# Performance work log

Measured on AMD Instinct MI355X. Metric: run time of the kernel, lower is better.

The kernel has to match this reference:

```python
import jax, jax.numpy as jnp
import numpy as np
import math

D_MODEL = 1024
N_HEADS = 16
HEAD_DIM = D_MODEL // N_HEADS

def setup_inputs() -> dict:
    key = jax.random.key(0)
    k1, k2, k3 = jax.random.split(key, 3)
    B, T = 4, 2048
    x = jax.random.normal(k1, (B, T, D_MODEL), dtype=jnp.float32)
    # weights stored as [in, out]; equivalent to torch Linear weight.T
    w_qkv = jax.random.normal(k2, (D_MODEL, 3 * D_MODEL), dtype=jnp.float32) * (1.0 / math.sqrt(D_MODEL))
    w_proj = jax.random.normal(k3, (D_MODEL, D_MODEL), dtype=jnp.float32) * (1.0 / math.sqrt(D_MODEL))
    return {"x": x, "w_qkv": w_qkv, "w_proj": w_proj}

def reference(x, w_qkv, w_proj):
    B, T, C = x.shape
    qkv = x @ w_qkv  # [B,T,3C]
    q, k, v = jnp.split(qkv, 3, axis=-1)
    # [B,T,C] -> [B,H,T,Dh]
    def to_heads(t):
        return t.reshape(B, T, N_HEADS, HEAD_DIM).transpose(0, 2, 1, 3)
    q, k, v = to_heads(q), to_heads(k), to_heads(v)
    scale = 1.0 / math.sqrt(HEAD_DIM)
    att = jnp.einsum('bhqd,bhkd->bhqk', q, k) * scale  # [B,H,T,T]
    causal = jnp.tril(jnp.ones((T, T), dtype=bool))
    att = jnp.where(causal[None, None], att, -jnp.inf)
    att = jax.nn.softmax(att, axis=-1)
    y = jnp.einsum('bhqk,bhkd->bhqd', att, v)  # [B,H,T,Dh]
    y = y.transpose(0, 2, 1, 3).reshape(B, T, C)
    return y @ w_proj
```

## Files before the change

### kernel.cpp

```cpp
#include <hip/hip_runtime.h>
#include <hip/hip_bf16.h>

typedef __bf16 bf16x8 __attribute__((ext_vector_type(8)));
typedef __bf16 bf16x4 __attribute__((ext_vector_type(4)));
typedef float  f32x4  __attribute__((ext_vector_type(4)));

#define MFMA16(a,b,c) __builtin_amdgcn_mfma_f32_16x16x32_bf16((a),(b),(c),0,0,0)

#define T_SEQ 2048
#define CDIM  1024
#define NH    16
#define DH    64
#define C3    3072
#define QKS   2048

#define GLDS(g, l) __builtin_amdgcn_global_load_lds( \
    (const __attribute__((address_space(1))) void*)(g), \
    (__attribute__((address_space(3))) void*)(l), 16, 0, 0)

__global__ void cast_f32_bf16_kernel(const float* __restrict__ in,
                                     __bf16* __restrict__ out, int n4) {
  int i = blockIdx.x * 256 + threadIdx.x;
  if (i >= n4) return;
  f32x4 v = ((const f32x4*)in)[i];
  bf16x4 o;
  o[0] = (__bf16)v[0]; o[1] = (__bf16)v[1];
  o[2] = (__bf16)v[2]; o[3] = (__bf16)v[3];
  ((bf16x4*)out)[i] = o;
}

__global__ void transpose_cast_kernel(const float* __restrict__ W,
                                      __bf16* __restrict__ WT, int R, int C,
                                      float qscale, int qcols) {
  __shared__ float tile[32][33];
  int c0 = blockIdx.x * 32, r0 = blockIdx.y * 32;
  int tx = threadIdx.x, ty = threadIdx.y;
#pragma unroll
  for (int i = 0; i < 32; i += 8)
    tile[ty + i][tx] = W[(size_t)(r0 + ty + i) * C + c0 + tx];
  __syncthreads();
#pragma unroll
  for (int i = 0; i < 32; i += 8) {
    int c = c0 + ty + i;
    float sc = (c < qcols) ? qscale : 1.0f;
    WT[(size_t)c * R + r0 + tx] = (__bf16)(tile[tx][ty + i] * sc);
  }
}

__global__ __launch_bounds__(256, 2)
void gemm1_kernel(const __bf16* __restrict__ A, const __bf16* __restrict__ BT,
                  __bf16* __restrict__ qkp, __bf16* __restrict__ VTp) {
  __shared__ __align__(16) __bf16 S[2][2][128 * 64];
  const int K = 1024;
  const int tid  = threadIdx.x;
  const int lane = tid & 63;
  const int g    = lane >> 4;
  const int l16  = lane & 15;
  const int wave = tid >> 6;
  const int wm   = wave >> 1;
  const int wn   = wave & 1;

  const int sb = (blockIdx.x & 7) * 192 + (blockIdx.x >> 3);
  const int bn = sb % 24;
  const int bm = sb / 24;

  const int srow = tid >> 3;
  const int scol = ((tid & 7) << 4) ^ ((srow & 7) << 4);
  const int swz  = (l16 & 7) << 4;

  const __bf16* Abase = A  + (size_t)(bm * 128 + srow) * K + (scol >> 1);
  const __bf16* Bbase = BT + (size_t)(bn * 128 + srow) * K + (scol >> 1);

  f32x4  acc[4][4] = {};
  bf16x8 ar[2][2];
  bf16x8 br[4][2];

#define STAGE_A(BUF, K0) do { \
    _Pragma("unroll") for (int u_ = 0; u_ < 4; ++u_) \
      GLDS(Abase + (size_t)u_ * 32 * K + (K0), (char*)&S[BUF][0][0] + u_ * 4096 + tid * 16); \
  } while (0)
#define STAGE_B(BUF, K0) do { \
    _Pragma("unroll") for (int u_ = 0; u_ < 4; ++u_) \
      GLDS(Bbase + (size_t)u_ * 32 * K + (K0), (char*)&S[BUF][1][0] + u_ * 4096 + tid * 16); \
  } while (0)

#define LDA(BUF, IH) do { \
    const char* ab_ = (const char*)&S[BUF][0][0]; \
    _Pragma("unroll") for (int i_ = 0; i_ < 2; ++i_) { \
      const char* rp_ = ab_ + (wm * 64 + (IH) * 32 + i_ * 16 + l16) * 128; \
      _Pragma("unroll") for (int kk_ = 0; kk_ < 2; ++kk_) \
        ar[i_][kk_] = *(const bf16x8*)(rp_ + ((kk_ * 64 + g * 16) ^ swz)); \
    } \
  } while (0)

#define LDB(BUF) do { \
    const char* bb_ = (const char*)&S[BUF][1][0]; \
    _Pragma("unroll") for (int j_ = 0; j_ < 4; ++j_) { \
      const char* rp_ = bb_ + (wn * 64 + j_ * 16 + l16) * 128; \
      _Pragma("unroll") for (int kk_ = 0; kk_ < 2; ++kk_) \
        br[j_][kk_] = *(const bf16x8*)(rp_ + ((kk_ * 64 + g * 16) ^ swz)); \
    } \
  } while (0)

#define MQ(IH) do { \
    __builtin_amdgcn_s_setprio(1); \
    _Pragma("unroll") for (int kk_ = 0; kk_ < 2; ++kk_) \
      _Pragma("unroll") for (int i_ = 0; i_ < 2; ++i_) \
        _Pragma("unroll") for (int j_ = 0; j_ < 4; ++j_) \
          acc[(IH) * 2 + i_][j_] = \
              MFMA16(ar[i_][kk_], br[j_][kk_], acc[(IH) * 2 + i_][j_]); \
    __builtin_amdgcn_s_setprio(0); \
  } while (0)

#define SBAR do { \
    __builtin_amdgcn_sched_barrier(0); \
    __builtin_amdgcn_s_barrier(); \
    __builtin_amdgcn_sched_barrier(0); \
  } while (0)

  STAGE_A(0, 0); STAGE_B(0, 0);
  asm volatile("s_waitcnt vmcnt(0)" ::: "memory");
  SBAR;

  const int NIT = K >> 7;
#pragma unroll 1
  for (int it = 0; it < NIT; ++it) {
    const int kt1 = (2 * it + 1) << 6;
    const int kt2 = (2 * it + 2) << 6;
    const bool stg = (it + 1) < NIT;

    LDA(0, 0); LDB(0);
    STAGE_A(1, kt1); STAGE_B(1, kt1);
    SBAR; MQ(0); SBAR;

    LDA(0, 1);
    asm volatile("s_waitcnt vmcnt(0)" ::: "memory");
    SBAR; MQ(1); SBAR;

    LDA(1, 0); LDB(1);
    if (stg) { STAGE_A(0, kt2); STAGE_B(0, kt2); }
    SBAR; MQ(0); SBAR;

    LDA(1, 1);
    asm volatile("s_waitcnt vmcnt(0)" ::: "memory");
    SBAR; MQ(1); SBAR;
  }

  if (bn < 16) {
#pragma unroll
    for (int a = 0; a < 4; ++a) {
      const int row0 = bm * 128 + wm * 64 + a * 16 + g * 4;
#pragma unroll
      for (int jj = 0; jj < 4; ++jj) {
        const int col = bn * 128 + wn * 64 + jj * 16 + l16;
#pragma unroll
        for (int r = 0; r < 4; ++r)
          qkp[(size_t)(row0 + r) * QKS + col] = (__bf16)acc[a][jj][r];
      }
    }
  } else {
#pragma unroll
    for (int a = 0; a < 4; ++a) {
      const int row0 = bm * 128 + wm * 64 + a * 16 + g * 4;
      const int b    = row0 >> 11;
      const int t0   = row0 & 2047;
#pragma unroll
      for (int jj = 0; jj < 4; ++jj) {
        const int c = (bn - 16) * 128 + wn * 64 + jj * 16 + l16;
        bf16x4 pb;
#pragma unroll
        for (int r = 0; r < 4; ++r) pb[r] = (__bf16)acc[a][jj][r];
        *(bf16x4*)(VTp + ((size_t)((b << 10) + c)) * T_SEQ + t0) = pb;
      }
    }
  }
#undef STAGE_A
#undef STAGE_B
#undef LDA
#undef LDB
#undef MQ
#undef SBAR
}

__global__ __launch_bounds__(512, 1)
void gemm2_kernel(const __bf16* __restrict__ A, const __bf16* __restrict__ BT,
                  float* __restrict__ Cout) {
  __shared__ __align__(16) __bf16 S[2][3][128 * 64];
  const int tid  = threadIdx.x;
  const int lane = tid & 63;
  const int g    = lane >> 4;
  const int l16  = lane & 15;
  const int wave = tid >> 6;
  const int wm   = wave >> 2;
  const int wn   = wave & 3;

  const int K = 1024;
  const int sb = (blockIdx.x & 7) * 32 + (blockIdx.x >> 3);
  const int bn = sb & 7;
  const int bm = sb >> 3;

  const int srow = tid >> 3;
  const int scol = ((tid & 7) << 4) ^ ((srow & 7) << 4);
  const int swz  = (l16 & 7) << 4;

  const __bf16* Abase = A  + (size_t)(bm * 256 + srow) * K + (scol >> 1);
  const __bf16* Bbase = BT + (size_t)(bn * 128 + srow) * K + (scol >> 1);

  f32x4  acc[8][2] = {};
  bf16x8 ar[4][2];
  bf16x8 br[2][2];

#define STAGE2(BUF, U, K0) do { \
    const __bf16* sp_ = ((U) < 2 ? Abase + (size_t)(U) * 128 * K : Bbase) + (K0); \
    char* dp_ = (char*)&S[BUF][U][0] + tid * 16; \
    GLDS(sp_, dp_); \
    GLDS(sp_ + (size_t)64 * K, dp_ + 8192); \
  } while (0)

#define LDA2(BUF, MH) do { \
    const char* ab_ = (const char*)&S[BUF][wm][0]; \
    _Pragma("unroll") for (int i_ = 0; i_ < 4; ++i_) { \
      const char* rp_ = ab_ + ((MH) * 64 + i_ * 16 + l16) * 128; \
      _Pragma("unroll") for (int kk_ = 0; kk_ < 2; ++kk_) \
        ar[i_][kk_] = *(const bf16x8*)(rp_ + ((kk_ * 64 + g * 16) ^ swz)); \
    } \
  } while (0)

#define LDB2(BUF) do { \
    const char* bb_ = (const char*)&S[BUF][2][0]; \
    _Pragma("unroll") for (int j_ = 0; j_ < 2; ++j_) { \
      const char* rp_ = bb_ + (wn * 32 + j_ * 16 + l16) * 128; \
      _Pragma("unroll") for (int kk_ = 0; kk_ < 2; ++kk_) \
        br[j_][kk_] = *(const bf16x8*)(rp_ + ((kk_ * 64 + g * 16) ^ swz)); \
    } \
  } while (0)

#define MQ2(MH) do { \
    __builtin_amdgcn_s_setprio(1); \
    _Pragma("unroll") for (int kk_ = 0; kk_ < 2; ++kk_) \
      _Pragma("unroll") for (int i_ = 0; i_ < 4; ++i_) \
        _Pragma("unroll") for (int j_ = 0; j_ < 2; ++j_) \
          acc[(MH) * 4 + i_][j_] = \
              MFMA16(ar[i_][kk_], br[j_][kk_], acc[(MH) * 4 + i_][j_]); \
    __builtin_amdgcn_s_setprio(0); \
  } while (0)

#define SBAR2 do { \
    __builtin_amdgcn_sched_barrier(0); \
    __builtin_amdgcn_s_barrier(); \
    __builtin_amdgcn_sched_barrier(0); \
  } while (0)

  STAGE2(0, 0, 0); STAGE2(0, 1, 0); STAGE2(0, 2, 0);
  STAGE2(1, 0, 64);
  asm volatile("s_waitcnt vmcnt(2)" ::: "memory");
  SBAR2;

  const int NIT = K >> 7;
#pragma unroll 1
  for (int it = 0; it < NIT; ++it) {
    const int k1 = (2 * it + 1) << 6;
    const int k2 = (2 * it + 2) << 6;
    const int k3 = (2 * it + 3) << 6;
    const bool stg = (it + 1) < NIT;

    LDA2(0, 0); LDB2(0);
    STAGE2(1, 1, k1); STAGE2(1, 2, k1);
    SBAR2; MQ2(0); SBAR2;

    LDA2(0, 1);
    if (stg) {
      STAGE2(0, 0, k2);
      asm volatile("s_waitcnt vmcnt(2)" ::: "memory");
    } else {
      asm volatile("s_waitcnt vmcnt(0)" ::: "memory");
    }
    SBAR2; MQ2(1); SBAR2;

    LDA2(1, 0); LDB2(1);
    if (stg) { STAGE2(0, 1, k2); STAGE2(0, 2, k2); }
    SBAR2; MQ2(0); SBAR2;

    LDA2(1, 1);
    if (stg) {
      STAGE2(1, 0, k3);
      asm volatile("s_waitcnt vmcnt(2)" ::: "memory");
    }
    SBAR2; MQ2(1); SBAR2;
  }

#pragma unroll
  for (int ii = 0; ii < 8; ++ii) {
    const int row0 = bm * 256 + wm * 128 + ii * 16 + g * 4;
#pragma unroll
    for (int jj = 0; jj < 2; ++jj) {
      const int col = bn * 128 + wn * 32 + jj * 16 + l16;
#pragma unroll
      for (int r = 0; r < 4; ++r)
        Cout[(size_t)(row0 + r) * 1024 + col] = acc[ii][jj][r];
    }
  }
#undef STAGE2
#undef LDA2
#undef LDB2
#undef MQ2
#undef SBAR2
}

__global__ __launch_bounds__(256)
void attn_kernel(const __bf16* __restrict__ qk, const __bf16* __restrict__ VT,
                 __bf16* __restrict__ y) {
  __shared__ __align__(16) __bf16 Klds[2][64 * 64];
  __shared__ __align__(16) __bf16 Vlds[2][64 * 64];
  __shared__ __align__(16) __bf16 Plds[4][32 * 64];
  const int tid  = threadIdx.x;
  const int lane = tid & 63;
  const int g    = lane >> 4;
  const int l16  = lane & 15;
  const int wave = tid >> 6;

  const int pairid = blockIdx.x >> 6;
  const int bh     = blockIdx.x & 63;
  const int h      = bh & (NH - 1);
  const int b      = bh >> 4;

  const __bf16* Qg = qk + (size_t)b * T_SEQ * QKS + h * DH;
  const __bf16* Kg = Qg + 1024;
  const __bf16* Vt = VT + ((size_t)(b << 10) + h * DH) * T_SEQ;

  const int srow = tid >> 3;
  const int scol = ((tid & 7) * 16) ^ ((srow & 7) << 4);
  const int swz  = (l16 & 7) << 4;

  const float NEG = -3.0e38f;

  bf16x8 ones;
#pragma unroll
  for (int j = 0; j < 8; ++j) ones[j] = (__bf16)1.0f;

  char* Pw = (char*)&Plds[wave][0];

#pragma unroll 1
  for (int ph = 0; ph < 2; ++ph) {
    const int qt    = ph ? (15 - pairid) : pairid;
    const int qbase = qt * 128 + wave * 32;

    bf16x8 qf[2][2];
#pragma unroll
    for (int qg = 0; qg < 2; ++qg)
#pragma unroll
      for (int kk = 0; kk < 2; ++kk)
        qf[qg][kk] = *(const bf16x8*)(Qg + (size_t)(qbase + qg * 16 + l16) * QKS + kk * 32 + g * 8);

    f32x4 o[2][4] = {};
    f32x4 o_l[2]  = {};

    const int nkb = 2 * qt + 2;
    {
      const __bf16* ksrc = Kg + (size_t)srow * QKS + (scol >> 1);
      GLDS(ksrc, (char*)&Klds[0][0] + tid * 16);
      GLDS(ksrc + (size_t)32 * QKS, (char*)&Klds[0][0] + 4096 + tid * 16);
      const __bf16* vsrc = Vt + (size_t)srow * T_SEQ + (scol >> 1);
      GLDS(vsrc, (char*)&Vlds[0][0] + tid * 16);
      GLDS(vsrc + (size_t)32 * T_SEQ, (char*)&Vlds[0][0] + 4096 + tid * 16);
    }
    __syncthreads();

    const __bf16* kstage = Kg + (size_t)(64 + srow) * QKS + (scol >> 1);
    const __bf16* vstage = Vt + (size_t)srow * T_SEQ + 64 + (scol >> 1);

#pragma unroll 1
    for (int kb = 0; kb < nkb; ++kb) {
      const int cur = kb & 1;
      if (kb + 1 < nkb) {
        GLDS(kstage, (char*)&Klds[cur ^ 1][0] + tid * 16);
        GLDS(kstage + (size_t)32 * QKS, (char*)&Klds[cur ^ 1][0] + 4096 + tid * 16);
        GLDS(vstage, (char*)&Vlds[cur ^ 1][0] + tid * 16);
        GLDS(vstage + (size_t)32 * T_SEQ, (char*)&Vlds[cur ^ 1][0] + 4096 + tid * 16);
        kstage += (size_t)64 * QKS;
        vstage += 64;
      }

      f32x4 s[2][4] = {};
      const char* Kb = (const char*)&Klds[cur][0];
#pragma unroll
      for (int kk = 0; kk < 2; ++kk) {
#pragma unroll
        for (int st = 0; st < 4; ++st) {
          const char* rowp = Kb + (st * 16 + l16) * 128;
          bf16x8 kf = *(const bf16x8*)(rowp + ((kk * 64 + g * 16) ^ swz));
          s[0][st] = MFMA16(kf, qf[0][kk], s[0][st]);
          s[1][st] = MFMA16(kf, qf[1][kk], s[1][st]);
        }
      }
      if (kb >= 2 * qt) {
        const int kvbase = (kb - 2 * qt) * 64;
#pragma unroll
        for (int qg = 0; qg < 2; ++qg) {
          const int qloc = wave * 32 + qg * 16 + l16;
#pragma unroll
          for (int st = 0; st < 4; ++st)
#pragma unroll
            for (int r = 0; r < 4; ++r)
              if (kvbase + st * 16 + g * 4 + r > qloc) s[qg][st][r] = NEG;
        }
      }
#pragma unroll
      for (int qg = 0; qg < 2; ++qg) {
        char* Pr = Pw + (qg * 16 + l16) * 128;
#pragma unroll
        for (int st = 0; st < 4; ++st) {
          bf16x4 pb;
#pragma unroll
          for (int r = 0; r < 4; ++r)
            pb[r] = (__bf16)__builtin_amdgcn_exp2f(s[qg][st][r]);
          *(bf16x4*)(Pr + ((st * 32 + g * 8) ^ swz)) = pb;
        }
      }

      const char* Vb = (const char*)&Vlds[cur][0];
#pragma unroll
      for (int hf = 0; hf < 2; ++hf) {
        bf16x8 pf0 = *(const bf16x8*)(Pw + (l16)       * 128 + ((hf * 64 + g * 16) ^ swz));
        bf16x8 pf1 = *(const bf16x8*)(Pw + (16 + l16)  * 128 + ((hf * 64 + g * 16) ^ swz));
        o_l[0] = MFMA16(ones, pf0, o_l[0]);
        o_l[1] = MFMA16(ones, pf1, o_l[1]);
#pragma unroll
        for (int dt = 0; dt < 4; ++dt) {
          bf16x8 vf = *(const bf16x8*)(Vb + (dt * 16 + l16) * 128 + ((hf * 64 + g * 16) ^ swz));
          o[0][dt] = MFMA16(vf, pf0, o[0][dt]);
          o[1][dt] = MFMA16(vf, pf1, o[1][dt]);
        }
      }
      __syncthreads();
    }

#pragma unroll
    for (int qg = 0; qg < 2; ++qg) {
      const float inv_l = 1.0f / o_l[qg][0];
      const int qrow = qbase + qg * 16 + l16;
#pragma unroll
      for (int dt = 0; dt < 4; ++dt)
#pragma unroll
        for (int r = 0; r < 4; ++r)
          y[((size_t)b * T_SEQ + qrow) * CDIM + h * DH + dt * 16 + g * 4 + r] =
              (__bf16)(o[qg][dt][r] * inv_l);
    }
  }
}

extern "C" void kernel_launch(void* const* d_in, const int* in_sizes, int n_in,
                              void* d_out, int out_size, void* d_ws, size_t ws_size,
                              hipStream_t stream) {
  const float* x      = (const float*)d_in[0];
  const float* w_qkv  = (const float*)d_in[1];
  const float* w_proj = (const float*)d_in[2];
  float* out = (float*)d_out;

  __bf16* xb     = (__bf16*)d_ws;
  __bf16* wqkvT  = xb + 8388608;
  __bf16* wprojT = wqkvT + 3145728;
  __bf16* qk     = wprojT + 1048576;
  __bf16* VT     = qk + 16777216;
  __bf16* yb     = VT + 8388608;

  const float SCF = 0.125f * 1.44269504088896340736f;

  cast_f32_bf16_kernel<<<8192, 256, 0, stream>>>(x, xb, 2097152);
  transpose_cast_kernel<<<dim3(96, 32), dim3(32, 8), 0, stream>>>(w_qkv, wqkvT, 1024, 3072, SCF, 1024);
  transpose_cast_kernel<<<dim3(32, 32), dim3(32, 8), 0, stream>>>(w_proj, wprojT, 1024, 1024, 1.0f, 0);
  gemm1_kernel<<<1536, 256, 0, stream>>>(xb, wqkvT, qk, VT);
  attn_kernel<<<512, 256, 0, stream>>>(qk, VT, yb);
  gemm2_kernel<<<256, 512, 0, stream>>>(yb, wprojT, out);
}
```

Baseline: 153.9 us.

## Software-pipeline attention loop: overlap QK/softmax of next block with PV of previous

Restructures the attention inner loop so that each iteration computes QK^T and exp for key block kb while doing the P·V product for block kb-1. V gets a triple buffer and P a per-wave double buffer so the two stages do not overwrite each other's data. The aim is to interleave the exp/VALU work with the MFMA work and hide LDS latency. In exchange it adds LDS usage (more shared memory per block, possibly lower occupancy) and a prologue/epilogue with extra barriers.

```diff
diff --git a/kernel.cpp b/kernel.cpp
--- a/kernel.cpp
+++ b/kernel.cpp
@@ -311,8 +311,8 @@
 void attn_kernel(const __bf16* __restrict__ qk, const __bf16* __restrict__ VT,
                  __bf16* __restrict__ y) {
   __shared__ __align__(16) __bf16 Klds[2][64 * 64];
-  __shared__ __align__(16) __bf16 Vlds[2][64 * 64];
-  __shared__ __align__(16) __bf16 Plds[4][32 * 64];
+  __shared__ __align__(16) __bf16 Vlds[3][64 * 64];
+  __shared__ __align__(16) __bf16 Plds[4][2][32 * 64];
   const int tid  = threadIdx.x;
   const int lane = tid & 63;
   const int g    = lane >> 4;
@@ -338,7 +338,62 @@
 #pragma unroll
   for (int j = 0; j < 8; ++j) ones[j] = (__bf16)1.0f;
 
-  char* Pw = (char*)&Plds[wave][0];
+#define STAGE_KV(T, KB, VB) do { \
+    const __bf16* ks_ = Kg + (size_t)((T) * 64 + srow) * QKS + (scol >> 1); \
+    GLDS(ks_, (char*)&Klds[KB][0] + tid * 16); \
+    GLDS(ks_ + (size_t)32 * QKS, (char*)&Klds[KB][0] + 4096 + tid * 16); \
+    const __bf16* vs_ = Vt + (size_t)srow * T_SEQ + (T) * 64 + (scol >> 1); \
+    GLDS(vs_, (char*)&Vlds[VB][0] + tid * 16); \
+    GLDS(vs_ + (size_t)32 * T_SEQ, (char*)&Vlds[VB][0] + 4096 + tid * 16); \
+  } while (0)
+
+#define QKSM(KB, PS, KB_IDX, QT) do { \
+    f32x4 s[2][4] = {}; \
+    const char* Kb_ = (const char*)&Klds[KB][0]; \
+    _Pragma("unroll") for (int kk = 0; kk < 2; ++kk) { \
+      _Pragma("unroll") for (int st = 0; st < 4; ++st) { \
+        const char* rowp = Kb_ + (st * 16 + l16) * 128; \
+        bf16x8 kf = *(const bf16x8*)(rowp + ((kk * 64 + g * 16) ^ swz)); \
+        s[0][st] = MFMA16(kf, qf[0][kk], s[0][st]); \
+        s[1][st] = MFMA16(kf, qf[1][kk], s[1][st]); \
+      } \
+    } \
+    if ((KB_IDX) >= 2 * (QT)) { \
+      const int kvbase = ((KB_IDX) - 2 * (QT)) * 64; \
+      _Pragma("unroll") for (int qg = 0; qg < 2; ++qg) { \
+        const int qloc = wave * 32 + qg * 16 + l16; \
+        _Pragma("unroll") for (int st = 0; st < 4; ++st) \
+          _Pragma("unroll") for (int r = 0; r < 4; ++r) \
+            if (kvbase + st * 16 + g * 4 + r > qloc) s[qg][st][r] = NEG; \
+      } \
+    } \
+    char* Pw_ = (char*)&Plds[wave][PS][0]; \
+    _Pragma("unroll") for (int qg = 0; qg < 2; ++qg) { \
+      char* Pr_ = Pw_ + (qg * 16 + l16) * 128; \
+      _Pragma("unroll") for (int st = 0; st < 4; ++st) { \
+        bf16x4 pb; \
+        _Pragma("unroll") for (int r = 0; r < 4; ++r) \
+          pb[r] = (__bf16)__builtin_amdgcn_exp2f(s[qg][st][r]); \
+        *(bf16x4*)(Pr_ + ((st * 32 + g * 8) ^ swz)) = pb; \
+      } \
+    } \
+  } while (0)
+
+#define PV(VB, PS) do { \
+    const char* Vb_ = (const char*)&Vlds[VB][0]; \
+    const char* Pw_ = (const char*)&Plds[wave][PS][0]; \
+    _Pragma("unroll") for (int hf = 0; hf < 2; ++hf) { \
+      bf16x8 pf0 = *(const bf16x8*)(Pw_ + (l16)      * 128 + ((hf * 64 + g * 16) ^ swz)); \
+      bf16x8 pf1 = *(const bf16x8*)(Pw_ + (16 + l16) * 128 + ((hf * 64 + g * 16) ^ swz)); \
+      o_l[0] = MFMA16(ones, pf0, o_l[0]); \
+      o_l[1] = MFMA16(ones, pf1, o_l[1]); \
+      _Pragma("unroll") for (int dt = 0; dt < 4; ++dt) { \
+        bf16x8 vf = *(const bf16x8*)(Vb_ + (dt * 16 + l16) * 128 + ((hf * 64 + g * 16) ^ swz)); \
+        o[0][dt] = MFMA16(vf, pf0, o[0][dt]); \
+        o[1][dt] = MFMA16(vf, pf1, o[1][dt]); \
+      } \
+    } \
+  } while (0)
 
 #pragma unroll 1
   for (int ph = 0; ph < 2; ++ph) {
@@ -356,84 +411,22 @@
     f32x4 o_l[2]  = {};
 
     const int nkb = 2 * qt + 2;
-    {
-      const __bf16* ksrc = Kg + (size_t)srow * QKS + (scol >> 1);
-      GLDS(ksrc, (char*)&Klds[0][0] + tid * 16);
-      GLDS(ksrc + (size_t)32 * QKS, (char*)&Klds[0][0] + 4096 + tid * 16);
-      const __bf16* vsrc = Vt + (size_t)srow * T_SEQ + (scol >> 1);
-      GLDS(vsrc, (char*)&Vlds[0][0] + tid * 16);
-      GLDS(vsrc + (size_t)32 * T_SEQ, (char*)&Vlds[0][0] + 4096 + tid * 16);
-    }
+
     __syncthreads();
-
-    const __bf16* kstage = Kg + (size_t)(64 + srow) * QKS + (scol >> 1);
-    const __bf16* vstage = Vt + (size_t)srow * T_SEQ + 64 + (scol >> 1);
+    STAGE_KV(0, 0, 0);
+    __syncthreads();
+    if (nkb > 1) STAGE_KV(1, 1, 1);
+    QKSM(0, 0, 0, qt);
+    __syncthreads();
 
 #pragma unroll 1
-    for (int kb = 0; kb < nkb; ++kb) {
-      const int cur = kb & 1;
-      if (kb + 1 < nkb) {
-        GLDS(kstage, (char*)&Klds[cur ^ 1][0] + tid * 16);
-        GLDS(kstage + (size_t)32 * QKS, (char*)&Klds[cur ^ 1][0] + 4096 + tid * 16);
-        GLDS(vstage, (char*)&Vlds[cur ^ 1][0] + tid * 16);
-        GLDS(vstage + (size_t)32 * T_SEQ, (char*)&Vlds[cur ^ 1][0] + 4096 + tid * 16);
-        kstage += (size_t)64 * QKS;
-        vstage += 64;
-      }
-
-      f32x4 s[2][4] = {};
-      const char* Kb = (const char*)&Klds[cur][0];
-#pragma unroll
-      for (int kk = 0; kk < 2; ++kk) {
-#pragma unroll
-        for (int st = 0; st < 4; ++st) {
-          const char* rowp = Kb + (st * 16 + l16) * 128;
-          bf16x8 kf = *(const bf16x8*)(rowp + ((kk * 64 + g * 16) ^ swz));
-          s[0][st] = MFMA16(kf, qf[0][kk], s[0][st]);
-          s[1][st] = MFMA16(kf, qf[1][kk], s[1][st]);
-        }
-      }
-      if (kb >= 2 * qt) {
-        const int kvbase = (kb - 2 * qt) * 64;
-#pragma unroll
-        for (int qg = 0; qg < 2; ++qg) {
-          const int qloc = wave * 32 + qg * 16 + l16;
-#pragma unroll
-          for (int st = 0; st < 4; ++st)
-#pragma unroll
-            for (int r = 0; r < 4; ++r)
-              if (kvbase + st * 16 + g * 4 + r > qloc) s[qg][st][r] = NEG;
-        }
-      }
-#pragma unroll
-      for (int qg = 0; qg < 2; ++qg) {
-        char* Pr = Pw + (qg * 16 + l16) * 128;
-#pragma unroll
-        for (int st = 0; st < 4; ++st) {
-          bf16x4 pb;
-#pragma unroll
-          for (int r = 0; r < 4; ++r)
-            pb[r] = (__bf16)__builtin_amdgcn_exp2f(s[qg][st][r]);
-          *(bf16x4*)(Pr + ((st * 32 + g * 8) ^ swz)) = pb;
-        }
-      }
-
-      const char* Vb = (const char*)&Vlds[cur][0];
-#pragma unroll
-      for (int hf = 0; hf < 2; ++hf) {
-        bf16x8 pf0 = *(const bf16x8*)(Pw + (l16)       * 128 + ((hf * 64 + g * 16) ^ swz));
-        bf16x8 pf1 = *(const bf16x8*)(Pw + (16 + l16)  * 128 + ((hf * 64 + g * 16) ^ swz));
-        o_l[0] = MFMA16(ones, pf0, o_l[0]);
-        o_l[1] = MFMA16(ones, pf1, o_l[1]);
-#pragma unroll
-        for (int dt = 0; dt < 4; ++dt) {
-          bf16x8 vf = *(const bf16x8*)(Vb + (dt * 16 + l16) * 128 + ((hf * 64 + g * 16) ^ swz));
-          o[0][dt] = MFMA16(vf, pf0, o[0][dt]);
-          o[1][dt] = MFMA16(vf, pf1, o[1][dt]);
-        }
-      }
+    for (int kb = 1; kb < nkb; ++kb) {
+      if (kb + 1 < nkb) STAGE_KV(kb + 1, (kb + 1) & 1, (kb + 1) % 3);
+      QKSM(kb & 1, kb & 1, kb, qt);
+      PV((kb - 1) % 3, (kb - 1) & 1);
       __syncthreads();
     }
+    PV((nkb - 1) % 3, (nkb - 1) & 1);
 
 #pragma unroll
     for (int qg = 0; qg < 2; ++qg) {
@@ -447,6 +440,9 @@
               (__bf16)(o[qg][dt][r] * inv_l);
     }
   }
+#undef STAGE_KV
+#undef QKSM
+#undef PV
 }
 
 extern "C" void kernel_launch(void* const* d_in, const int* in_sizes, int n_in,
```

Result: no change. 153.6 us (-0.2%).
